# Kernel optimization log

Measured on AMD Instinct MI355X. Metric: run time of the kernel, lower is better.

The kernel has to match this reference:

```python
import jax, jax.numpy as jnp
import numpy as np

B, L, H = 1, 2048, 2048          # batch, seq_len, hidden_size
E, N, K, R = 4096, 16, 4, 128    # intermediate, ssm_state, conv_kernel, dt_rank


def setup_inputs() -> dict:
    key = jax.random.key(0)
    ks = jax.random.split(key, 8)
    s = 0.02
    inp = {
        "hidden_states": jax.random.normal(ks[0], (B, L, H), jnp.float32),
        "in_proj_w": jax.random.normal(ks[1], (2 * E, H), jnp.float32) * s,
        "conv_w": jax.random.normal(ks[2], (E, 1, K), jnp.float32) * s,
        "conv_b": jax.random.normal(ks[3], (E,), jnp.float32) * s,
        "x_proj_w": jax.random.normal(ks[4], (R + 2 * N, E), jnp.float32) * s,
        "dt_proj_w": jax.random.normal(ks[5], (E, R), jnp.float32) * s,
        "dt_proj_b": jax.random.normal(ks[6], (E,), jnp.float32) * s,
        "A_log": jnp.broadcast_to(jnp.log(jnp.arange(1, N + 1, dtype=jnp.float32))[None, :], (E, N)).copy(),
        "D": jnp.ones((E,), jnp.float32),
        "out_proj_w": jax.random.normal(ks[7], (H, E), jnp.float32) * s,
    }
    return inp


def _mamba_mixer(hidden_states, in_proj_w, conv_w, conv_b, x_proj_w,
                 dt_proj_w, dt_proj_b, A_log, D, out_proj_w):
    # in_proj -> [B, L, 2E], split into hidden / gate
    proj = jnp.einsum('blh,eh->ble', hidden_states, in_proj_w)
    h, gate = jnp.split(proj, 2, axis=-1)            # each [B, L, E]

    # depthwise causal conv1d over time, padding K-1 on the left
    h_c = h.transpose(0, 2, 1)                       # [B, E, L]
    h_c = jax.lax.conv_general_dilated(
        h_c, conv_w, window_strides=(1,), padding=[(K - 1, 0)],
        feature_group_count=E, dimension_numbers=('NCH', 'OIH', 'NCH'))
    h_c = h_c + conv_b[None, :, None]
    h = jax.nn.silu(h_c).transpose(0, 2, 1)          # [B, L, E]

    # x_proj -> dt, B, C (input-dependent SSM params)
    ssm = jnp.einsum('ble,pe->blp', h, x_proj_w)     # [B, L, R+2N]
    dt, Bp, Cp = jnp.split(ssm, [R, R + N], axis=-1)
    dt = jax.nn.softplus(jnp.einsum('blr,er->ble', dt, dt_proj_w) + dt_proj_b)  # [B,L,E]

    A = -jnp.exp(A_log)                              # [E, N]
    dA = jnp.exp(dt[..., None] * A)                  # [B, L, E, N]
    dBu = (dt * h)[..., None] * Bp[:, :, None, :]    # [B, L, E, N]

    # selective scan: s_t = dA_t * s_{t-1} + dBu_t
    def step(s, xs):
        dA_t, dBu_t = xs
        s = s * dA_t + dBu_t
        return s, s

    s0 = jnp.zeros((h.shape[0], E, N), h.dtype)
    _, states = jax.lax.scan(step, s0, (dA.transpose(1, 0, 2, 3), dBu.transpose(1, 0, 2, 3)))
    # states: [L, B, E, N]
    y = jnp.einsum('lben,bln->ble', states, Cp)      # [B, L, E]
    y = y + h * D                                    # skip via D
    y = y * jax.nn.silu(gate)                        # gated output
    return jnp.einsum('ble,he->blh', y, out_proj_w)  # [B, L, H]


def reference(hidden_states, in_proj_w, conv_w, conv_b, x_proj_w,
              dt_proj_w, dt_proj_b, A_log, D, out_proj_w):
    return _mamba_mixer(hidden_states, in_proj_w, conv_w, conv_b, x_proj_w,
                        dt_proj_w, dt_proj_b, A_log, D, out_proj_w)
```

## Files before the change

### kernel.cpp

```cpp
#include <hip/hip_runtime.h>

#define LL 2048
#define HH 2048
#define EE 4096
#define NS 16
#define RR 128
#define CT 32
#define NC (LL / CT)
#define BM 128
#define BN 128
#define BK 64

typedef __bf16 bf16x8 __attribute__((ext_vector_type(8)));
typedef float f32x4 __attribute__((ext_vector_type(4)));

__device__ __forceinline__ unsigned short f2bf(float f) {
  union { float f; unsigned int u; } v; v.f = f;
  unsigned int r = v.u + 0x7fffu + ((v.u >> 16) & 1u);
  return (unsigned short)(r >> 16);
}

__device__ __forceinline__ float bf2f(unsigned short u) {
  union { unsigned int i; float f; } v;
  v.i = ((unsigned int)u) << 16;
  return v.f;
}

__device__ __forceinline__ float softplus_fast(float x) {
  if (x > 20.0f) return x;
  float e = __builtin_amdgcn_exp2f(1.44269504f * x);
  return 0.69314718f * __builtin_amdgcn_logf(1.0f + e);
}

__device__ __forceinline__ void async_cp16(const unsigned short* g,
                                           unsigned short* l) {
  __builtin_amdgcn_global_load_lds(
      (const __attribute__((address_space(1))) unsigned int*)g,
      (__attribute__((address_space(3))) unsigned int*)l, 16, 0, 0);
}

__global__ void cast_bf16_k(const float* __restrict__ in,
                            unsigned short* __restrict__ out, int n4) {
  int i = blockIdx.x * blockDim.x + threadIdx.x;
  if (i >= n4) return;
  float4 v = reinterpret_cast<const float4*>(in)[i];
  ushort4 o;
  o.x = f2bf(v.x); o.y = f2bf(v.y); o.z = f2bf(v.z); o.w = f2bf(v.w);
  reinterpret_cast<ushort4*>(out)[i] = o;
}

__global__ void zero_k(float* __restrict__ p, int n4) {
  int i = blockIdx.x * blockDim.x + threadIdx.x;
  if (i >= n4) return;
  float4 z; z.x = z.y = z.z = z.w = 0.0f;
  reinterpret_cast<float4*>(p)[i] = z;
}

template <int EPI>
__global__ __launch_bounds__(512, 2) void gemm256(
    const unsigned short* __restrict__ A,
    const unsigned short* __restrict__ B,
    float* __restrict__ C,
    int M, int N, int K, int tilesM, int splitk,
    float* __restrict__ auxF, unsigned short* __restrict__ auxB) {
  __shared__ __align__(16) unsigned short As[2][16384];
  __shared__ __align__(16) unsigned short Bs[2][16384];

  int bid = blockIdx.x;
  int tnInner = bid & 7;
  int rest = bid >> 3;
  int tm = rest % tilesM;
  int tn = (rest / tilesM) * 8 + tnInner;

  int Kslice = K / splitk;
  int k_begin = blockIdx.y * Kslice;
  int NT = Kslice / 64;

  int tid = threadIdx.x;
  int lane = tid & 63;
  int wave = tid >> 6;
  int wm = wave >> 2;
  int wn = wave & 3;
  int m16 = lane & 15, quad = lane >> 4;

  const unsigned short* Ab = A + (size_t)tm * 256 * K;
  const unsigned short* Bb = B + (size_t)tn * 256 * K;

  int rowS = tid >> 3;
  int gcbS = (tid & 7) ^ (rowS & 7);
  int ldsWB = (tid & ~63) * 8;

  int sw = m16 & 7;
  int coff0 = (quad ^ sw) << 3;
  int coff1 = ((4 + quad) ^ sw) << 3;
  int aoff = (wm * 128 + m16) * 64;
  int boff = (wn * 64 + m16) * 64;

  f32x4 acc[8][4];
#pragma unroll
  for (int i = 0; i < 8; ++i)
#pragma unroll
    for (int j = 0; j < 4; ++j)
#pragma unroll
      for (int t = 0; t < 4; ++t) acc[i][j][t] = 0.0f;

#pragma unroll
  for (int c = 0; c < 4; ++c)
    async_cp16(Ab + (size_t)(c * 64 + rowS) * K + k_begin + gcbS * 8,
               &As[0][c * 4096 + ldsWB]);
#pragma unroll
  for (int c = 0; c < 4; ++c)
    async_cp16(Bb + (size_t)(c * 64 + rowS) * K + k_begin + gcbS * 8,
               &Bs[0][c * 4096 + ldsWB]);
  asm volatile("s_waitcnt vmcnt(0)" ::: "memory");
  __builtin_amdgcn_s_barrier();

  auto tile_body = [&](int t, int buf) {
    unsigned short* Acur = &As[buf][0];
    unsigned short* Bcur = &Bs[buf][0];
    if (t + 1 < NT) {
      unsigned short* An = &As[buf ^ 1][0];
      unsigned short* Bn = &Bs[buf ^ 1][0];
      int kt = k_begin + (t + 1) * 64;
#pragma unroll
      for (int c = 0; c < 4; ++c)
        async_cp16(Ab + (size_t)(c * 64 + rowS) * K + kt + gcbS * 8,
                   An + c * 4096 + ldsWB);
#pragma unroll
      for (int c = 0; c < 4; ++c)
        async_cp16(Bb + (size_t)(c * 64 + rowS) * K + kt + gcbS * 8,
                   Bn + c * 4096 + ldsWB);
    }

    bf16x8 a[4][2], b0[2][2], b1[2][2];

#pragma unroll
    for (int i = 0; i < 4; ++i) {
      a[i][0] = *reinterpret_cast<const bf16x8*>(&Acur[aoff + i * 1024 + coff0]);
      a[i][1] = *reinterpret_cast<const bf16x8*>(&Acur[aoff + i * 1024 + coff1]);
    }
#pragma unroll
    for (int j = 0; j < 2; ++j) {
      b0[j][0] = *reinterpret_cast<const bf16x8*>(&Bcur[boff + j * 1024 + coff0]);
      b0[j][1] = *reinterpret_cast<const bf16x8*>(&Bcur[boff + j * 1024 + coff1]);
    }
    __builtin_amdgcn_s_barrier();
    asm volatile("s_waitcnt lgkmcnt(0)" ::: "memory");
    __builtin_amdgcn_sched_barrier(0);
    __builtin_amdgcn_s_setprio(1);
#pragma unroll
    for (int i = 0; i < 4; ++i)
#pragma unroll
      for (int j = 0; j < 2; ++j) {
        acc[i][j] = __builtin_amdgcn_mfma_f32_16x16x32_bf16(a[i][0], b0[j][0], acc[i][j], 0, 0, 0);
        acc[i][j] = __builtin_amdgcn_mfma_f32_16x16x32_bf16(a[i][1], b0[j][1], acc[i][j], 0, 0, 0);
      }
    __builtin_amdgcn_s_setprio(0);
    __builtin_amdgcn_s_barrier();

#pragma unroll
    for (int j = 0; j < 2; ++j) {
      b1[j][0] = *reinterpret_cast<const bf16x8*>(&Bcur[boff + (2 + j) * 1024 + coff0]);
      b1[j][1] = *reinterpret_cast<const bf16x8*>(&Bcur[boff + (2 + j) * 1024 + coff1]);
    }
    __builtin_amdgcn_s_barrier();
    asm volatile("s_waitcnt lgkmcnt(0)" ::: "memory");
    __builtin_amdgcn_sched_barrier(0);
    __builtin_amdgcn_s_setprio(1);
#pragma unroll
    for (int i = 0; i < 4; ++i)
#pragma unroll
      for (int j = 0; j < 2; ++j) {
        acc[i][2 + j] = __builtin_amdgcn_mfma_f32_16x16x32_bf16(a[i][0], b1[j][0], acc[i][2 + j], 0, 0, 0);
        acc[i][2 + j] = __builtin_amdgcn_mfma_f32_16x16x32_bf16(a[i][1], b1[j][1], acc[i][2 + j], 0, 0, 0);
      }
    __builtin_amdgcn_s_setprio(0);
    __builtin_amdgcn_s_barrier();

#pragma unroll
    for (int i = 0; i < 4; ++i) {
      a[i][0] = *reinterpret_cast<const bf16x8*>(&Acur[aoff + (4 + i) * 1024 + coff0]);
      a[i][1] = *reinterpret_cast<const bf16x8*>(&Acur[aoff + (4 + i) * 1024 + coff1]);
    }
    __builtin_amdgcn_s_barrier();
    asm volatile("s_waitcnt lgkmcnt(0)" ::: "memory");
    __builtin_amdgcn_sched_barrier(0);
    __builtin_amdgcn_s_setprio(1);
#pragma unroll
    for (int i = 0; i < 4; ++i)
#pragma unroll
      for (int j = 0; j < 2; ++j) {
        acc[4 + i][2 + j] = __builtin_amdgcn_mfma_f32_16x16x32_bf16(a[i][0], b1[j][0], acc[4 + i][2 + j], 0, 0, 0);
        acc[4 + i][2 + j] = __builtin_amdgcn_mfma_f32_16x16x32_bf16(a[i][1], b1[j][1], acc[4 + i][2 + j], 0, 0, 0);
      }
    __builtin_amdgcn_s_setprio(0);
    __builtin_amdgcn_s_barrier();

    __builtin_amdgcn_s_setprio(1);
#pragma unroll
    for (int i = 0; i < 4; ++i)
#pragma unroll
      for (int j = 0; j < 2; ++j) {
        acc[4 + i][j] = __builtin_amdgcn_mfma_f32_16x16x32_bf16(a[i][0], b0[j][0], acc[4 + i][j], 0, 0, 0);
        acc[4 + i][j] = __builtin_amdgcn_mfma_f32_16x16x32_bf16(a[i][1], b0[j][1], acc[4 + i][j], 0, 0, 0);
      }
    __builtin_amdgcn_s_setprio(0);
    asm volatile("s_waitcnt vmcnt(0)" ::: "memory");
    __builtin_amdgcn_s_barrier();
  };

  for (int t = 0; t < NT; t += 2) {
    tile_body(t, 0);
    tile_body(t + 1, 1);
  }

  int rowB = tm * 256 + wm * 128;
  int colB = tn * 256 + wn * 64;
  if constexpr (EPI == 1) {
#pragma unroll
    for (int mi = 0; mi < 8; ++mi)
#pragma unroll
      for (int nj = 0; nj < 4; ++nj) {
        int col = colB + nj * 16 + m16;
        int row0 = rowB + mi * 16 + quad * 4;
#pragma unroll
        for (int t4 = 0; t4 < 4; ++t4)
          atomicAdd(&C[(size_t)(row0 + t4) * N + col], acc[mi][nj][t4]);
      }
  } else {
    if (colB < EE) {
#pragma unroll
      for (int mi = 0; mi < 8; ++mi)
#pragma unroll
        for (int nj = 0; nj < 4; ++nj) {
          int col = colB + nj * 16 + m16;
          int row0 = rowB + mi * 16 + quad * 4;
#pragma unroll
          for (int t4 = 0; t4 < 4; ++t4)
            auxF[(size_t)(row0 + t4) * EE + col] = acc[mi][nj][t4];
        }
    } else {
#pragma unroll
      for (int mi = 0; mi < 8; ++mi)
#pragma unroll
        for (int nj = 0; nj < 4; ++nj) {
          int cg = colB + nj * 16 + m16 - EE;
          int row0 = rowB + mi * 16 + quad * 4;
#pragma unroll
          for (int t4 = 0; t4 < 4; ++t4) {
            float v = acc[mi][nj][t4];
            float s = v / (1.0f + __expf(-v));
            auxB[(size_t)(row0 + t4) * EE + cg] = f2bf(s);
          }
        }
    }
  }
}

template <int EPI>
__global__ __launch_bounds__(256) void gemm_lds_t(
    const unsigned short* __restrict__ A,
    const unsigned short* __restrict__ B,
    float* __restrict__ C,
    int M, int N, int K, int tilesM, int splitk,
    const float* __restrict__ bias, float* __restrict__ auxF,
    unsigned short* __restrict__ auxB) {
  __shared__ __align__(16) unsigned short As[BM * BK];
  __shared__ __align__(16) unsigned short Bs[BN * BK];

  int bid = blockIdx.x;
  int tnInner = bid & 7;
  int rest = bid >> 3;
  int tm = rest % tilesM;
  int tnOuter = rest / tilesM;
  int tn = tnOuter * 8 + tnInner;

  int Kslice = K / splitk;
  int k_begin = blockIdx.y * Kslice;
  int k_end = k_begin + Kslice;

  int tid = threadIdx.x;
  int lane = tid & 63;
  int wave = tid >> 6;
  int wm = wave & 1, wn = wave >> 1;
  int m16 = lane & 15, quad = lane >> 4;

  const unsigned short* Ab = A + (size_t)tm * BM * K;
  const unsigned short* Bb = B + (size_t)tn * BN * K;

  int srow[4], sgcb[4];
#pragma unroll
  for (int it = 0; it < 4; ++it) {
    int blk = it * 256 + tid;
    srow[it] = blk >> 3;
    sgcb[it] = (blk & 7) ^ (srow[it] & 7);
  }
  int ldsbase = (tid & ~63) * 8;

  f32x4 acc[4][4];
#pragma unroll
  for (int i = 0; i < 4; ++i)
#pragma unroll
    for (int j = 0; j < 4; ++j)
#pragma unroll
      for (int t = 0; t < 4; ++t) acc[i][j][t] = 0.0f;

  for (int k0 = k_begin; k0 < k_end; k0 += BK) {
    __syncthreads();
#pragma unroll
    for (int it = 0; it < 4; ++it)
      async_cp16(Ab + (size_t)srow[it] * K + k0 + sgcb[it] * 8,
                 &As[it * 2048 + ldsbase]);
#pragma unroll
    for (int it = 0; it < 4; ++it)
      async_cp16(Bb + (size_t)srow[it] * K + k0 + sgcb[it] * 8,
                 &Bs[it * 2048 + ldsbase]);
    __syncthreads();
#pragma unroll
    for (int kk = 0; kk < 2; ++kk) {
      bf16x8 a[4], b[4];
#pragma unroll
      for (int i = 0; i < 4; ++i) {
        int rr = wm * 64 + i * 16 + m16;
        int cb = (kk << 2) + quad;
        a[i] = *reinterpret_cast<const bf16x8*>(
            &As[rr * BK + ((cb ^ (rr & 7)) << 3)]);
      }
#pragma unroll
      for (int j = 0; j < 4; ++j) {
        int rr = wn * 64 + j * 16 + m16;
        int cb = (kk << 2) + quad;
        b[j] = *reinterpret_cast<const bf16x8*>(
            &Bs[rr * BK + ((cb ^ (rr & 7)) << 3)]);
      }
#pragma unroll
      for (int i = 0; i < 4; ++i)
#pragma unroll
        for (int j = 0; j < 4; ++j)
          acc[i][j] =
              __builtin_amdgcn_mfma_f32_16x16x32_bf16(a[i], b[j], acc[i][j], 0, 0, 0);
    }
  }

  int rowB = tm * BM + wm * 64;
  int colB = tn * BN + wn * 64;
  if constexpr (EPI == 1) {
#pragma unroll
    for (int i = 0; i < 4; ++i)
#pragma unroll
      for (int j = 0; j < 4; ++j) {
        int col = colB + j * 16 + m16;
        int row0 = rowB + i * 16 + quad * 4;
#pragma unroll
        for (int t = 0; t < 4; ++t)
          atomicAdd(&C[(size_t)(row0 + t) * N + col], acc[i][j][t]);
      }
  } else {
#pragma unroll
    for (int i = 0; i < 4; ++i)
#pragma unroll
      for (int j = 0; j < 4; ++j) {
        int col = colB + j * 16 + m16;
        float bv = bias[col];
        int row0 = rowB + i * 16 + quad * 4;
#pragma unroll
        for (int t = 0; t < 4; ++t) {
          float x = acc[i][j][t] + bv;
          auxB[(size_t)(row0 + t) * EE + col] = f2bf(softplus_fast(x));
        }
      }
  }
}

__global__ __launch_bounds__(256) void gemm_bt(
    const unsigned short* __restrict__ A,
    const unsigned short* __restrict__ B,
    float* __restrict__ C,
    int M, int N, int K, int tilesN, int splitk) {
  int bid = blockIdx.x;
  int groupSize = 8 * tilesN;
  int g = bid / groupSize, r = bid % groupSize;
  int tm = g * 8 + (r & 7);
  int tn = r >> 3;

  int Kslice = K / splitk;
  int k_begin = blockIdx.y * Kslice;
  int k_end = k_begin + Kslice;

  int tid = threadIdx.x;
  int wave = tid >> 6, lane = tid & 63;
  int wm = wave & 1, wn = wave >> 1;
  int m16 = lane & 15, quad = lane >> 4;
  int rowBase = tm * 64 + wm * 32;
  int colBase = tn * 128 + wn * 64;

  const unsigned short* a0p = A + (size_t)(rowBase + m16) * K + quad * 8;
  const unsigned short* a1p = A + (size_t)(rowBase + 16 + m16) * K + quad * 8;
  const unsigned short* bp[4];
  bool bok[4];
#pragma unroll
  for (int j = 0; j < 4; ++j) {
    int col = colBase + j * 16 + m16;
    bok[j] = (col < N);
    bp[j] = B + (size_t)(bok[j] ? col : 0) * K + quad * 8;
  }

  f32x4 acc[2][4];
#pragma unroll
  for (int i = 0; i < 2; ++i)
#pragma unroll
    for (int j = 0; j < 4; ++j)
#pragma unroll
      for (int t = 0; t < 4; ++t) acc[i][j][t] = 0.0f;

  bf16x8 zero8;
#pragma unroll
  for (int t = 0; t < 8; ++t) zero8[t] = (__bf16)0.0f;

  for (int k = k_begin; k < k_end; k += 32) {
    bf16x8 a0 = *reinterpret_cast<const bf16x8*>(a0p + k);
    bf16x8 a1 = *reinterpret_cast<const bf16x8*>(a1p + k);
    bf16x8 b[4];
#pragma unroll
    for (int j = 0; j < 4; ++j)
      b[j] = bok[j] ? *reinterpret_cast<const bf16x8*>(bp[j] + k) : zero8;
#pragma unroll
    for (int j = 0; j < 4; ++j) {
      acc[0][j] = __builtin_amdgcn_mfma_f32_16x16x32_bf16(a0, b[j], acc[0][j], 0, 0, 0);
      acc[1][j] = __builtin_amdgcn_mfma_f32_16x16x32_bf16(a1, b[j], acc[1][j], 0, 0, 0);
    }
  }

#pragma unroll
  for (int i = 0; i < 2; ++i)
#pragma unroll
    for (int j = 0; j < 4; ++j) {
      int col = colBase + j * 16 + m16;
      if (col >= N) continue;
      int row0 = rowBase + i * 16 + quad * 4;
      if (splitk == 1) {
#pragma unroll
        for (int t = 0; t < 4; ++t)
          C[(size_t)(row0 + t) * N + col] = acc[i][j][t];
      } else {
#pragma unroll
        for (int t = 0; t < 4; ++t)
          atomicAdd(&C[(size_t)(row0 + t) * N + col], acc[i][j][t]);
      }
    }
}

__global__ __launch_bounds__(256) void conv_silu_k(
    const float* __restrict__ projh, const float* __restrict__ cw,
    const float* __restrict__ cb, unsigned short* __restrict__ hb) {
  int e = blockIdx.x * 256 + threadIdx.x;
  int l0 = blockIdx.y * 16;
  float w0 = cw[e * 4 + 0], w1 = cw[e * 4 + 1];
  float w2 = cw[e * 4 + 2], w3 = cw[e * 4 + 3];
  float bias = cb[e];
  float xm3 = (l0 >= 3) ? projh[(size_t)(l0 - 3) * EE + e] : 0.0f;
  float xm2 = (l0 >= 2) ? projh[(size_t)(l0 - 2) * EE + e] : 0.0f;
  float xm1 = (l0 >= 1) ? projh[(size_t)(l0 - 1) * EE + e] : 0.0f;
#pragma unroll
  for (int t = 0; t < 16; ++t) {
    int l = l0 + t;
    float x0 = projh[(size_t)l * EE + e];
    float acc = bias + w0 * xm3 + w1 * xm2 + w2 * xm1 + w3 * x0;
    float s = acc / (1.0f + __expf(-acc));
    hb[(size_t)l * EE + e] = f2bf(s);
    xm3 = xm2; xm2 = xm1; xm1 = x0;
  }
}

__global__ void dtcast_k(const float* __restrict__ ssm,
                         unsigned short* __restrict__ dtin, int n) {
  int i = blockIdx.x * blockDim.x + threadIdx.x;
  if (i >= n) return;
  int l = i >> 7, r = i & 127;
  dtin[i] = f2bf(ssm[l * 160 + r]);
}

__global__ __launch_bounds__(256) void scan_partA(
    const unsigned short* __restrict__ dtb, const unsigned short* __restrict__ hb,
    const float* __restrict__ ssm, const float* __restrict__ A_log,
    float* __restrict__ P, float* __restrict__ S) {
  int e = blockIdx.y * 256 + threadIdx.x;
  int c = blockIdx.x;
  float Aa[16];
#pragma unroll
  for (int q = 0; q < 4; ++q) {
    float4 a = reinterpret_cast<const float4*>(&A_log[(size_t)e * NS])[q];
    Aa[q * 4 + 0] = -__expf(a.x) * 1.44269504f;
    Aa[q * 4 + 1] = -__expf(a.y) * 1.44269504f;
    Aa[q * 4 + 2] = -__expf(a.z) * 1.44269504f;
    Aa[q * 4 + 3] = -__expf(a.w) * 1.44269504f;
  }
  float s[16], p[16];
#pragma unroll
  for (int n = 0; n < 16; ++n) { s[n] = 0.0f; p[n] = 1.0f; }
  int l0 = c * CT;
#pragma unroll 2
  for (int t = 0; t < CT; ++t) {
    int l = l0 + t;
    size_t o = (size_t)l * EE + e;
    float dtv = bf2f(dtb[o]);
    float hv = bf2f(hb[o]);
    float Bv[16];
#pragma unroll
    for (int q = 0; q < 4; ++q)
      *reinterpret_cast<float4*>(&Bv[q * 4]) =
          reinterpret_cast<const float4*>(&ssm[(size_t)l * 160 + 128])[q];
    float z = dtv * hv;
#pragma unroll
    for (int n = 0; n < 16; ++n) {
      float dA = __builtin_amdgcn_exp2f(dtv * Aa[n]);
      s[n] = s[n] * dA + z * Bv[n];
      p[n] *= dA;
    }
  }
  size_t base = ((size_t)c * EE + e) * NS;
#pragma unroll
  for (int q = 0; q < 4; ++q) {
    reinterpret_cast<float4*>(&P[base])[q] = *reinterpret_cast<float4*>(&p[q * 4]);
    reinterpret_cast<float4*>(&S[base])[q] = *reinterpret_cast<float4*>(&s[q * 4]);
  }
}

__global__ __launch_bounds__(256) void scan_chunkB(
    const float* __restrict__ P, float* __restrict__ S) {
  int gidx = blockIdx.x * 256 + threadIdx.x;
  float s = 0.0f;
  float pv = P[gidx], sv = S[gidx];
  for (int c = 0; c < NC; ++c) {
    float pn = 0.0f, sn = 0.0f;
    if (c + 1 < NC) {
      size_t i2 = (size_t)(c + 1) * (EE * NS) + gidx;
      pn = P[i2];
      sn = S[i2];
    }
    float s_next = s * pv + sv;
    S[(size_t)c * (EE * NS) + gidx] = s;
    s = s_next;
    pv = pn; sv = sn;
  }
}

__global__ __launch_bounds__(256) void scan_partC(
    const unsigned short* __restrict__ dtb, const unsigned short* __restrict__ hb,
    const float* __restrict__ ssm, const float* __restrict__ A_log,
    const float* __restrict__ Dp, const unsigned short* __restrict__ sg,
    const float* __restrict__ Sinit, unsigned short* __restrict__ yb) {
  int e = blockIdx.y * 256 + threadIdx.x;
  int c = blockIdx.x;
  float Aa[16];
#pragma unroll
  for (int q = 0; q < 4; ++q) {
    float4 a = reinterpret_cast<const float4*>(&A_log[(size_t)e * NS])[q];
    Aa[q * 4 + 0] = -__expf(a.x) * 1.44269504f;
    Aa[q * 4 + 1] = -__expf(a.y) * 1.44269504f;
    Aa[q * 4 + 2] = -__expf(a.z) * 1.44269504f;
    Aa[q * 4 + 3] = -__expf(a.w) * 1.44269504f;
  }
  float Dv = Dp[e];
  float s[16];
  size_t base = ((size_t)c * EE + e) * NS;
#pragma unroll
  for (int q = 0; q < 4; ++q)
    *reinterpret_cast<float4*>(&s[q * 4]) =
        reinterpret_cast<const float4*>(&Sinit[base])[q];
  int l0 = c * CT;
#pragma unroll 2
  for (int t = 0; t < CT; ++t) {
    int l = l0 + t;
    size_t o = (size_t)l * EE + e;
    float dtv = bf2f(dtb[o]);
    float hv = bf2f(hb[o]);
    float Bv[16], Cv[16];
#pragma unroll
    for (int q = 0; q < 4; ++q) {
      *reinterpret_cast<float4*>(&Bv[q * 4]) =
          reinterpret_cast<const float4*>(&ssm[(size_t)l * 160 + 128])[q];
      *reinterpret_cast<float4*>(&Cv[q * 4]) =
          reinterpret_cast<const float4*>(&ssm[(size_t)l * 160 + 144])[q];
    }
    float z = dtv * hv;
    float y = 0.0f;
#pragma unroll
    for (int n = 0; n < 16; ++n) {
      float dA = __builtin_amdgcn_exp2f(dtv * Aa[n]);
      s[n] = s[n] * dA + z * Bv[n];
      y += s[n] * Cv[n];
    }
    float gv = bf2f(sg[o]);
    float yv = (y + hv * Dv) * gv;
    yb[o] = f2bf(yv);
  }
}

extern "C" void kernel_launch(void* const* d_in, const int* in_sizes, int n_in,
                              void* d_out, int out_size, void* d_ws, size_t ws_size,
                              hipStream_t stream) {
  const float* hs   = (const float*)d_in[0];
  const float* w1   = (const float*)d_in[1];
  const float* cw   = (const float*)d_in[2];
  const float* cb   = (const float*)d_in[3];
  const float* xw   = (const float*)d_in[4];
  const float* dtw  = (const float*)d_in[5];
  const float* dtb  = (const float*)d_in[6];
  const float* Alog = (const float*)d_in[7];
  const float* Dp   = (const float*)d_in[8];
  const float* ow   = (const float*)d_in[9];
  float* out = (float*)d_out;

  char* ws = (char*)d_ws;
  size_t off = 0;
  auto alloc = [&](size_t b) {
    char* p = ws + off;
    off += (b + 255) & ~(size_t)255;
    return p;
  };
  float* projh = (float*)alloc((size_t)LL * EE * 4);
  unsigned short* sg  = (unsigned short*)alloc((size_t)LL * EE * 2);
  unsigned short* hb  = (unsigned short*)alloc((size_t)LL * EE * 2);
  unsigned short* dtb_buf = (unsigned short*)alloc((size_t)LL * EE * 2);
  unsigned short* w1b = (unsigned short*)alloc((size_t)2 * EE * HH * 2);
  unsigned short* hsb = (unsigned short*)alloc((size_t)LL * HH * 2);
  unsigned short* yb  = (unsigned short*)alloc((size_t)LL * EE * 2);
  unsigned short* owb = (unsigned short*)alloc((size_t)HH * EE * 2);
  unsigned short* xwb = (unsigned short*)alloc((size_t)160 * EE * 2);
  float* ssm = (float*)alloc((size_t)LL * 160 * 4);
  unsigned short* dtin = (unsigned short*)alloc((size_t)LL * RR * 2);
  unsigned short* dtwb = (unsigned short*)alloc((size_t)EE * RR * 2);
  float* Pbuf = (float*)alloc((size_t)NC * EE * NS * 4);
  float* Sbuf = (float*)alloc((size_t)NC * EE * NS * 4);

  auto cast = [&](const float* in, unsigned short* o, int nelem) {
    int n4 = nelem / 4;
    cast_bf16_k<<<(n4 + 255) / 256, 256, 0, stream>>>(in, o, n4);
  };
  cast(hs, hsb, LL * HH);
  cast(w1, w1b, 2 * EE * HH);
  cast(xw, xwb, 160 * EE);
  cast(dtw, dtwb, EE * RR);
  cast(ow, owb, HH * EE);
  zero_k<<<(LL * 160 / 4 + 255) / 256, 256, 0, stream>>>(ssm, LL * 160 / 4);
  zero_k<<<(LL * HH / 4 + 255) / 256, 256, 0, stream>>>(out, LL * HH / 4);

  {
    int tilesM = LL / 256;
    int tilesN = (2 * EE) / 256;
    gemm256<2><<<dim3(tilesM * tilesN, 1), 512, 0, stream>>>(
        hsb, w1b, nullptr, LL, 2 * EE, HH, tilesM, 1, projh, sg);
  }
  conv_silu_k<<<dim3(EE / 256, LL / 16), 256, 0, stream>>>(projh, cw, cb, hb);
  {
    int tilesN = (160 + 127) / 128, tilesM = LL / 64;
    gemm_bt<<<dim3(tilesM * tilesN, 8), 256, 0, stream>>>(
        hb, xwb, ssm, LL, 160, EE, tilesN, 8);
  }
  dtcast_k<<<(LL * RR + 255) / 256, 256, 0, stream>>>(ssm, dtin, LL * RR);
  {
    int tilesN = EE / BN, tilesM = LL / BM;
    gemm_lds_t<4><<<dim3(tilesM * tilesN, 1), 256, 0, stream>>>(
        dtin, dtwb, nullptr, LL, EE, RR, tilesM, 1, dtb, nullptr, dtb_buf);
  }
  scan_partA<<<dim3(NC, EE / 256), 256, 0, stream>>>(dtb_buf, hb, ssm, Alog,
                                                     Pbuf, Sbuf);
  scan_chunkB<<<EE * NS / 256, 256, 0, stream>>>(Pbuf, Sbuf);
  scan_partC<<<dim3(NC, EE / 256), 256, 0, stream>>>(dtb_buf, hb, ssm, Alog, Dp,
                                                     sg, Sbuf, yb);
  {
    int tilesM = LL / 256, tilesN = HH / 256;
    gemm256<1><<<dim3(tilesM * tilesN, 4), 512, 0, stream>>>(
        yb, owb, out, LL, HH, EE, tilesM, 4, nullptr, nullptr);
  }
}
```

Before: 469.4 us.

## Interleave half-tile async prefetches across MFMA phases in gemm256; switch out_proj GEMM

```diff
diff --git a/kernel.cpp b/kernel.cpp
--- a/kernel.cpp
+++ b/kernel.cpp
@@ -104,114 +104,208 @@
 #pragma unroll
       for (int t = 0; t < 4; ++t) acc[i][j][t] = 0.0f;
 
-#pragma unroll
-  for (int c = 0; c < 4; ++c)
-    async_cp16(Ab + (size_t)(c * 64 + rowS) * K + k_begin + gcbS * 8,
-               &As[0][c * 4096 + ldsWB]);
-#pragma unroll
-  for (int c = 0; c < 4; ++c)
-    async_cp16(Bb + (size_t)(c * 64 + rowS) * K + k_begin + gcbS * 8,
-               &Bs[0][c * 4096 + ldsWB]);
-  asm volatile("s_waitcnt vmcnt(0)" ::: "memory");
+  auto stageA = [&](int bufb, int t, int h) {
+    int kt = k_begin + t * 64;
+    unsigned short* dst = &As[bufb][0];
+#pragma unroll
+    for (int c = 2 * h; c < 2 * h + 2; ++c)
+      async_cp16(Ab + (size_t)(c * 64 + rowS) * K + kt + gcbS * 8,
+                 dst + c * 4096 + ldsWB);
+  };
+  auto stageB = [&](int bufb, int t, int h) {
+    int kt = k_begin + t * 64;
+    unsigned short* dst = &Bs[bufb][0];
+#pragma unroll
+    for (int c = 2 * h; c < 2 * h + 2; ++c)
+      async_cp16(Bb + (size_t)(c * 64 + rowS) * K + kt + gcbS * 8,
+                 dst + c * 4096 + ldsWB);
+  };
+
+  stageA(0, 0, 0); stageA(0, 0, 1);
+  stageB(0, 0, 0); stageB(0, 0, 1);
+  stageB(1, 1, 0); stageB(1, 1, 1);
+  stageA(1, 1, 0);
+  asm volatile("s_waitcnt vmcnt(6)" ::: "memory");
   __builtin_amdgcn_s_barrier();
 
-  auto tile_body = [&](int t, int buf) {
-    unsigned short* Acur = &As[buf][0];
-    unsigned short* Bcur = &Bs[buf][0];
-    if (t + 1 < NT) {
-      unsigned short* An = &As[buf ^ 1][0];
-      unsigned short* Bn = &Bs[buf ^ 1][0];
-      int kt = k_begin + (t + 1) * 64;
-#pragma unroll
-      for (int c = 0; c < 4; ++c)
-        async_cp16(Ab + (size_t)(c * 64 + rowS) * K + kt + gcbS * 8,
-                   An + c * 4096 + ldsWB);
-#pragma unroll
-      for (int c = 0; c < 4; ++c)
-        async_cp16(Bb + (size_t)(c * 64 + rowS) * K + kt + gcbS * 8,
-                   Bn + c * 4096 + ldsWB);
-    }
-
-    bf16x8 a[4][2], b0[2][2], b1[2][2];
+  bf16x8 a[4][2], b0[2][2], b1[2][2];
+
+  for (int t0 = 0; t0 < NT; t0 += 2) {
+    int t1 = t0 + 1;
+    bool notLast = (t0 + 2 < NT);
+    unsigned short* A0 = &As[0][0];
+    unsigned short* B0 = &Bs[0][0];
+    unsigned short* A1 = &As[1][0];
+    unsigned short* B1 = &Bs[1][0];
 
 #pragma unroll
     for (int i = 0; i < 4; ++i) {
-      a[i][0] = *reinterpret_cast<const bf16x8*>(&Acur[aoff + i * 1024 + coff0]);
-      a[i][1] = *reinterpret_cast<const bf16x8*>(&Acur[aoff + i * 1024 + coff1]);
+      a[i][0] = *reinterpret_cast<const bf16x8*>(&A0[aoff + i * 1024 + coff0]);
+      a[i][1] = *reinterpret_cast<const bf16x8*>(&A0[aoff + i * 1024 + coff1]);
     }
 #pragma unroll
     for (int j = 0; j < 2; ++j) {
-      b0[j][0] = *reinterpret_cast<const bf16x8*>(&Bcur[boff + j * 1024 + coff0]);
-      b0[j][1] = *reinterpret_cast<const bf16x8*>(&Bcur[boff + j * 1024 + coff1]);
-    }
+      b0[j][0] = *reinterpret_cast<const bf16x8*>(&B0[boff + j * 1024 + coff0]);
+      b0[j][1] = *reinterpret_cast<const bf16x8*>(&B0[boff + j * 1024 + coff1]);
+    }
+    stageA(1, t1, 1);
     __builtin_amdgcn_s_barrier();
     asm volatile("s_waitcnt lgkmcnt(0)" ::: "memory");
     __builtin_amdgcn_sched_barrier(0);
     __builtin_amdgcn_s_setprio(1);
 #pragma unroll
-    for (int i = 0; i < 4; ++i)
-#pragma unroll
-      for (int j = 0; j < 2; ++j) {
-        acc[i][j] = __builtin_amdgcn_mfma_f32_16x16x32_bf16(a[i][0], b0[j][0], acc[i][j], 0, 0, 0);
-        acc[i][j] = __builtin_amdgcn_mfma_f32_16x16x32_bf16(a[i][1], b0[j][1], acc[i][j], 0, 0, 0);
-      }
+    for (int kk = 0; kk < 2; ++kk)
+#pragma unroll
+      for (int i = 0; i < 4; ++i)
+#pragma unroll
+        for (int j = 0; j < 2; ++j)
+          acc[i][j] = __builtin_amdgcn_mfma_f32_16x16x32_bf16(
+              a[i][kk], b0[j][kk], acc[i][j], 0, 0, 0);
     __builtin_amdgcn_s_setprio(0);
     __builtin_amdgcn_s_barrier();
 
 #pragma unroll
     for (int j = 0; j < 2; ++j) {
-      b1[j][0] = *reinterpret_cast<const bf16x8*>(&Bcur[boff + (2 + j) * 1024 + coff0]);
-      b1[j][1] = *reinterpret_cast<const bf16x8*>(&Bcur[boff + (2 + j) * 1024 + coff1]);
+      b1[j][0] = *reinterpret_cast<const bf16x8*>(&B0[boff + (2 + j) * 1024 + coff0]);
+      b1[j][1] = *reinterpret_cast<const bf16x8*>(&B0[boff + (2 + j) * 1024 + coff1]);
     }
     __builtin_amdgcn_s_barrier();
     asm volatile("s_waitcnt lgkmcnt(0)" ::: "memory");
     __builtin_amdgcn_sched_barrier(0);
     __builtin_amdgcn_s_setprio(1);
 #pragma unroll
-    for (int i = 0; i < 4; ++i)
-#pragma unroll
-      for (int j = 0; j < 2; ++j) {
-        acc[i][2 + j] = __builtin_amdgcn_mfma_f32_16x16x32_bf16(a[i][0], b1[j][0], acc[i][2 + j], 0, 0, 0);
-        acc[i][2 + j] = __builtin_amdgcn_mfma_f32_16x16x32_bf16(a[i][1], b1[j][1], acc[i][2 + j], 0, 0, 0);
-      }
+    for (int kk = 0; kk < 2; ++kk)
+#pragma unroll
+      for (int i = 0; i < 4; ++i)
+#pragma unroll
+        for (int j = 0; j < 2; ++j)
+          acc[i][2 + j] = __builtin_amdgcn_mfma_f32_16x16x32_bf16(
+              a[i][kk], b1[j][kk], acc[i][2 + j], 0, 0, 0);
     __builtin_amdgcn_s_setprio(0);
     __builtin_amdgcn_s_barrier();
 
 #pragma unroll
     for (int i = 0; i < 4; ++i) {
-      a[i][0] = *reinterpret_cast<const bf16x8*>(&Acur[aoff + (4 + i) * 1024 + coff0]);
-      a[i][1] = *reinterpret_cast<const bf16x8*>(&Acur[aoff + (4 + i) * 1024 + coff1]);
-    }
+      a[i][0] = *reinterpret_cast<const bf16x8*>(&A0[aoff + (4 + i) * 1024 + coff0]);
+      a[i][1] = *reinterpret_cast<const bf16x8*>(&A0[aoff + (4 + i) * 1024 + coff1]);
+    }
+    if (notLast) stageB(0, t0 + 2, 0);
     __builtin_amdgcn_s_barrier();
     asm volatile("s_waitcnt lgkmcnt(0)" ::: "memory");
     __builtin_amdgcn_sched_barrier(0);
     __builtin_amdgcn_s_setprio(1);
 #pragma unroll
-    for (int i = 0; i < 4; ++i)
-#pragma unroll
-      for (int j = 0; j < 2; ++j) {
-        acc[4 + i][2 + j] = __builtin_amdgcn_mfma_f32_16x16x32_bf16(a[i][0], b1[j][0], acc[4 + i][2 + j], 0, 0, 0);
-        acc[4 + i][2 + j] = __builtin_amdgcn_mfma_f32_16x16x32_bf16(a[i][1], b1[j][1], acc[4 + i][2 + j], 0, 0, 0);
-      }
+    for (int kk = 0; kk < 2; ++kk)
+#pragma unroll
+      for (int i = 0; i < 4; ++i)
+#pragma unroll
+        for (int j = 0; j < 2; ++j)
+          acc[4 + i][2 + j] = __builtin_amdgcn_mfma_f32_16x16x32_bf16(
+              a[i][kk], b1[j][kk], acc[4 + i][2 + j], 0, 0, 0);
     __builtin_amdgcn_s_setprio(0);
     __builtin_amdgcn_s_barrier();
 
+    if (notLast) stageB(0, t0 + 2, 1);
     __builtin_amdgcn_s_setprio(1);
 #pragma unroll
-    for (int i = 0; i < 4; ++i)
-#pragma unroll
-      for (int j = 0; j < 2; ++j) {
-        acc[4 + i][j] = __builtin_amdgcn_mfma_f32_16x16x32_bf16(a[i][0], b0[j][0], acc[4 + i][j], 0, 0, 0);
-        acc[4 + i][j] = __builtin_amdgcn_mfma_f32_16x16x32_bf16(a[i][1], b0[j][1], acc[4 + i][j], 0, 0, 0);
-      }
+    for (int kk = 0; kk < 2; ++kk)
+#pragma unroll
+      for (int i = 0; i < 4; ++i)
+#pragma unroll
+        for (int j = 0; j < 2; ++j)
+          acc[4 + i][j] = __builtin_amdgcn_mfma_f32_16x16x32_bf16(
+              a[i][kk], b0[j][kk], acc[4 + i][j], 0, 0, 0);
     __builtin_amdgcn_s_setprio(0);
-    asm volatile("s_waitcnt vmcnt(0)" ::: "memory");
-    __builtin_amdgcn_s_barrier();
-  };
-
-  for (int t = 0; t < NT; t += 2) {
-    tile_body(t, 0);
-    tile_body(t + 1, 1);
+    if (notLast) {
+      asm volatile("s_waitcnt vmcnt(4)" ::: "memory");
+    } else {
+      asm volatile("s_waitcnt vmcnt(0)" ::: "memory");
+    }
+    __builtin_amdgcn_s_barrier();
+
+#pragma unroll
+    for (int i = 0; i < 4; ++i) {
+      a[i][0] = *reinterpret_cast<const bf16x8*>(&A1[aoff + i * 1024 + coff0]);
+      a[i][1] = *reinterpret_cast<const bf16x8*>(&A1[aoff + i * 1024 + coff1]);
+    }
+#pragma unroll
+    for (int j = 0; j < 2; ++j) {
+      b0[j][0] = *reinterpret_cast<const bf16x8*>(&B1[boff + j * 1024 + coff0]);
+      b0[j][1] = *reinterpret_cast<const bf16x8*>(&B1[boff + j * 1024 + coff1]);
+    }
+    if (notLast) stageA(0, t0 + 2, 0);
+    __builtin_amdgcn_s_barrier();
+    asm volatile("s_waitcnt lgkmcnt(0)" ::: "memory");
+    __builtin_amdgcn_sched_barrier(0);
+    __builtin_amdgcn_s_setprio(1);
+#pragma unroll
+    for (int kk = 0; kk < 2; ++kk)
+#pragma unroll
+      for (int i = 0; i < 4; ++i)
+#pragma unroll
+        for (int j = 0; j < 2; ++j)
+          acc[i][j] = __builtin_amdgcn_mfma_f32_16x16x32_bf16(
+              a[i][kk], b0[j][kk], acc[i][j], 0, 0, 0);
+    __builtin_amdgcn_s_setprio(0);
+    __builtin_amdgcn_s_barrier();
+
+#pragma unroll
+    for (int j = 0; j < 2; ++j) {
+      b1[j][0] = *reinterpret_cast<const bf16x8*>(&B1[boff + (2 + j) * 1024 + coff0]);
+      b1[j][1] = *reinterpret_cast<const bf16x8*>(&B1[boff + (2 + j) * 1024 + coff1]);
+    }
+    if (notLast) stageA(0, t0 + 2, 1);
+    __builtin_amdgcn_s_barrier();
+    asm volatile("s_waitcnt lgkmcnt(0)" ::: "memory");
+    __builtin_amdgcn_sched_barrier(0);
+    __builtin_amdgcn_s_setprio(1);
+#pragma unroll
+    for (int kk = 0; kk < 2; ++kk)
+#pragma unroll
+      for (int i = 0; i < 4; ++i)
+#pragma unroll
+        for (int j = 0; j < 2; ++j)
+          acc[i][2 + j] = __builtin_amdgcn_mfma_f32_16x16x32_bf16(
+              a[i][kk], b1[j][kk], acc[i][2 + j], 0, 0, 0);
+    __builtin_amdgcn_s_setprio(0);
+    __builtin_amdgcn_s_barrier();
+
+#pragma unroll
+    for (int i = 0; i < 4; ++i) {
+      a[i][0] = *reinterpret_cast<const bf16x8*>(&A1[aoff + (4 + i) * 1024 + coff0]);
+      a[i][1] = *reinterpret_cast<const bf16x8*>(&A1[aoff + (4 + i) * 1024 + coff1]);
+    }
+    if (notLast) stageB(1, t1 + 2, 0);
+    __builtin_amdgcn_s_barrier();
+    asm volatile("s_waitcnt lgkmcnt(0)" ::: "memory");
+    __builtin_amdgcn_sched_barrier(0);
+    __builtin_amdgcn_s_setprio(1);
+#pragma unroll
+    for (int kk = 0; kk < 2; ++kk)
+#pragma unroll
+      for (int i = 0; i < 4; ++i)
+#pragma unroll
+        for (int j = 0; j < 2; ++j)
+          acc[4 + i][2 + j] = __builtin_amdgcn_mfma_f32_16x16x32_bf16(
+              a[i][kk], b1[j][kk], acc[4 + i][2 + j], 0, 0, 0);
+    __builtin_amdgcn_s_setprio(0);
+    __builtin_amdgcn_s_barrier();
+
+    if (notLast) { stageB(1, t1 + 2, 1); stageA(1, t1 + 2, 0); }
+    __builtin_amdgcn_s_setprio(1);
+#pragma unroll
+    for (int kk = 0; kk < 2; ++kk)
+#pragma unroll
+      for (int i = 0; i < 4; ++i)
+#pragma unroll
+        for (int j = 0; j < 2; ++j)
+          acc[4 + i][j] = __builtin_amdgcn_mfma_f32_16x16x32_bf16(
+              a[i][kk], b0[j][kk], acc[4 + i][j], 0, 0, 0);
+    __builtin_amdgcn_s_setprio(0);
+    if (notLast) {
+      asm volatile("s_waitcnt vmcnt(6)" ::: "memory");
+    }
+    __builtin_amdgcn_s_barrier();
   }
 
   int rowB = tm * 256 + wm * 128;
@@ -670,8 +764,8 @@
   scan_partC<<<dim3(NC, EE / 256), 256, 0, stream>>>(dtb_buf, hb, ssm, Alog, Dp,
                                                      sg, Sbuf, yb);
   {
-    int tilesM = LL / 256, tilesN = HH / 256;
-    gemm256<1><<<dim3(tilesM * tilesN, 4), 512, 0, stream>>>(
-        yb, owb, out, LL, HH, EE, tilesM, 4, nullptr, nullptr);
-  }
-}
+    int tilesN = HH / BN, tilesM = LL / BM;
+    gemm_lds_t<1><<<dim3(tilesM * tilesN, 2), 256, 0, stream>>>(
+        yb, owb, out, LL, HH, EE, tilesM, 2, nullptr, nullptr, nullptr);
+  }
+}
```

Measured after the change: 419.6 us. 10.6% less time.
